# Performance work log

Hardware: AMD Instinct MI355X
Metric: run time of the kernel (lower is better)

## Reference

```python
import jax, jax.numpy as jnp
import numpy as np

C, K, D_LLM = 32, 16, 768
B, L, D_MODEL = 8, 512, 256
H, D_KEYS = 8, 32
TEMP = 1.0 / np.sqrt(D_KEYS)


def setup_inputs() -> dict:
    key = jax.random.key(0)
    ks = jax.random.split(key, 8)
    topk = jax.random.normal(ks[0], (C, K, D_LLM), dtype=jnp.float32)
    ts_emb = jax.random.normal(ks[1], (B, L, D_MODEL), dtype=jnp.float32)
    probs = jax.random.uniform(ks[2], (B, L, C), dtype=jnp.float32)
    probs = probs / jnp.sum(probs, axis=-1, keepdims=True)  # soft cluster probabilities
    scale = 0.02  # keep pre-softmax logits in a stable range
    q_proj = jax.random.normal(ks[3], (C, H * D_KEYS, D_MODEL + 1), dtype=jnp.float32) * scale
    k_proj = jax.random.normal(ks[4], (C, H * D_KEYS, D_LLM + 1), dtype=jnp.float32) * scale
    v_proj = jax.random.normal(ks[5], (C, H * D_KEYS, D_LLM + 1), dtype=jnp.float32) * scale
    out_w = jax.random.normal(ks[6], (C, H, D_KEYS, D_LLM), dtype=jnp.float32) * scale
    out_b = jax.random.normal(ks[7], (C, D_LLM), dtype=jnp.float32) * scale
    return {"topk_token_embeddings": topk, "ts_emb": ts_emb, "cluster_probs": probs,
            "q_proj": q_proj, "k_proj": k_proj, "v_proj": v_proj,
            "out_w": out_w, "out_b": out_b}


def reference(topk_token_embeddings, ts_emb, cluster_probs, q_proj, k_proj, v_proj, out_w, out_b):
    b, l, _ = ts_emb.shape
    c, k, d_llm = topk_token_embeddings.shape
    # per-cluster Q/K/V projections (weights have an extra trailing bias column)
    q = jnp.einsum('bld,cgd->blcg', ts_emb, q_proj[..., :-1]) + q_proj[..., -1]
    q = q.reshape(b, l, c, H, D_KEYS)
    kk = jnp.einsum('ckd,cgd->kcg', topk_token_embeddings, k_proj[..., :-1]) + k_proj[..., -1]
    kk = kk.reshape(k, c, H, D_KEYS)
    v = jnp.einsum('ckd,cgd->kcg', topk_token_embeddings, v_proj[..., :-1]) + v_proj[..., -1]
    v = v.reshape(k, c, H, D_KEYS)
    # cross attention over the k retrieved tokens, per cluster and head
    att = jnp.einsum('blchd,kchd->bchlk', q, kk)  # (B,c,H,L,k)
    att = jax.nn.softmax(TEMP * att, axis=-1)  # dropout disabled (eval)
    out_v = jnp.einsum('bchlk,kchd->bclhd', att, v)
    aligned = jnp.einsum('bclhd,chde->blce', out_v, out_w) + out_b  # (B,L,c,d_llm)
    fused = jnp.sum(aligned * cluster_probs[:, :, :, None], axis=-2)  # (B,L,d_llm)
    return fused
```

## Files before the change

### kernel.cpp

```cpp
#include <hip/hip_runtime.h>
#include <hip/hip_bf16.h>

#define C_   32
#define K_   16
#define DLLM 768
#define DM   256
#define H_   8
#define DK   32
#define G_   256
#define BL   4096
#define NN   4096
#define E_   768
#define LDP  4160
#define TEMPF 0.17677669529663687f
#define SCL2  0.2550348647f

typedef __attribute__((ext_vector_type(8))) short bf16x8;
typedef __attribute__((ext_vector_type(4))) float f32x4;
typedef unsigned int u32;

__device__ __forceinline__ unsigned short f2bf(float f) {
    unsigned int u = __float_as_uint(f);
    unsigned int r = (u + 0x7fffu + ((u >> 16) & 1u)) >> 16;
    return (unsigned short)r;
}
__device__ __forceinline__ float bf2f(unsigned int u) {
    return __uint_as_float(u << 16);
}

__device__ __forceinline__ void gl16(const void* g, void* l) {
    __builtin_amdgcn_global_load_lds(
        (const __attribute__((address_space(1))) u32*)g,
        (__attribute__((address_space(3))) u32*)l, 16, 0, 0);
}

__global__ __launch_bounds__(256) void k1_kv(const float* __restrict__ topk,
                                             const float* __restrict__ kp,
                                             const float* __restrict__ vp,
                                             float* __restrict__ partk,
                                             float* __restrict__ partv) {
    const int c  = blockIdx.x;
    const int dc = blockIdx.y;
    const int d0 = dc * 96;
    const int g  = threadIdx.x;
    __shared__ float t_l[K_][96];
    for (int i = threadIdx.x; i < 384; i += 256) {
        int k = i / 24, c4 = (i % 24) * 4;
        *reinterpret_cast<float4*>(&t_l[k][c4]) =
            *reinterpret_cast<const float4*>(topk + (size_t)(c * K_ + k) * DLLM + d0 + c4);
    }
    __syncthreads();
    const float* kpr = kp + (size_t)(c * G_ + g) * (DLLM + 1) + d0;
    const float* vpr = vp + (size_t)(c * G_ + g) * (DLLM + 1) + d0;
    float acck[K_] = {}, accv[K_] = {};
    for (int d = 0; d < 96; d += 4) {
        float4 wk4 = *reinterpret_cast<const float4*>(kpr + d);
        float4 wv4 = *reinterpret_cast<const float4*>(vpr + d);
        const float wk[4] = {wk4.x, wk4.y, wk4.z, wk4.w};
        const float wv[4] = {wv4.x, wv4.y, wv4.z, wv4.w};
#pragma unroll
        for (int dd = 0; dd < 4; ++dd)
#pragma unroll
            for (int k = 0; k < K_; ++k) {
                acck[k] += wk[dd] * t_l[k][d + dd];
                accv[k] += wv[dd] * t_l[k][d + dd];
            }
    }
    float* pk = partk + ((size_t)(c * 8 + dc) * K_) * G_ + g;
    float* pv = partv + ((size_t)(c * 8 + dc) * K_) * G_ + g;
#pragma unroll
    for (int k = 0; k < K_; ++k) {
        pk[k * G_] = acck[k];
        pv[k * G_] = accv[k];
    }
}

__global__ __launch_bounds__(256) void k1r0(const float* __restrict__ partk,
                                            const float* __restrict__ partv,
                                            const float* __restrict__ kp,
                                            const float* __restrict__ vp,
                                            float* __restrict__ kk,
                                            float* __restrict__ vv,
                                            const float* __restrict__ ts,
                                            const float* __restrict__ probs,
                                            const float* __restrict__ outb,
                                            unsigned short* __restrict__ tsb,
                                            unsigned short* __restrict__ P,
                                            unsigned short* __restrict__ VWt) {
    const int bid0 = blockIdx.x, t = threadIdx.x;
    if (bid0 < 512) {
        const int idx = bid0 * 256 + t;
        const int g = idx & 255, rest = idx >> 8;
        const int k = rest & 15, c = rest >> 4;
        float sk = kp[(size_t)(c * G_ + g) * (DLLM + 1) + DLLM];
        float sv = vp[(size_t)(c * G_ + g) * (DLLM + 1) + DLLM];
#pragma unroll
        for (int dc = 0; dc < 8; ++dc) {
            sk += partk[((size_t)(c * 8 + dc) * K_ + k) * G_ + g];
            sv += partv[((size_t)(c * 8 + dc) * K_ + k) * G_ + g];
        }
        kk[idx] = sk;
        vv[idx] = sv;
        return;
    }
    const int bid = bid0 - 512;
    if (bid < 1024) {
        const int idx = bid * 1024 + t * 4;
        float4 v = *reinterpret_cast<const float4*>(ts + idx);
        uint2 o;
        o.x = f2bf(v.x) | ((unsigned)f2bf(v.y) << 16);
        o.y = f2bf(v.z) | ((unsigned)f2bf(v.w) << 16);
        *reinterpret_cast<uint2*>(tsb + idx) = o;
    } else if (bid < 1056) {
        const int b2 = bid - 1024;
        const int row = b2 * 128 + (t >> 1);
        const int ch = (t & 1) * 16;
        unsigned short o[16];
#pragma unroll
        for (int j = 0; j < 16; ++j) o[j] = f2bf(probs[row * 32 + ch + j]);
        uint4 u0, u1;
        u0.x = o[0] | (o[1] << 16);  u0.y = o[2] | (o[3] << 16);
        u0.z = o[4] | (o[5] << 16);  u0.w = o[6] | (o[7] << 16);
        u1.x = o[8] | (o[9] << 16);  u1.y = o[10] | (o[11] << 16);
        u1.z = o[12] | (o[13] << 16); u1.w = o[14] | (o[15] << 16);
        unsigned short* dst = P + (size_t)row * LDP + 4096 + ch;
        *reinterpret_cast<uint4*>(dst) = u0;
        *reinterpret_cast<uint4*>(dst + 8) = u1;
        uint4 z = {0u, 0u, 0u, 0u};
        unsigned short* pz = P + (size_t)row * LDP + 4128 + ch;
        *reinterpret_cast<uint4*>(pz) = z;
        *reinterpret_cast<uint4*>(pz + 8) = z;
    } else {
        const int idx = (bid - 1056) * 256 + t;
        const int e = idx >> 5, cc = idx & 31;
        VWt[(size_t)e * LDP + 4096 + cc] = f2bf(outb[cc * E_ + e]);
        VWt[(size_t)e * LDP + 4128 + cc] = 0;
    }
}

__global__ __launch_bounds__(768) void k23(const float* __restrict__ qp,
                                           const float* __restrict__ kk,
                                           const float* __restrict__ ow,
                                           const float* __restrict__ vv,
                                           unsigned short* __restrict__ A2t,
                                           float* __restrict__ abias,
                                           unsigned short* __restrict__ VWt) {
    const int c = blockIdx.x, h = blockIdx.y;
    const int t = threadIdx.x;
    __shared__ float kk_l[K_][DK];
    __shared__ float v_l[K_][DK];
    __shared__ float bq_l[DK];
    if (t < 512) {
        int k = t / DK, d = t % DK;
        kk_l[k][d] = kk[(size_t)(c * K_ + k) * G_ + h * DK + d];
        v_l[k][d]  = vv[(size_t)(c * K_ + k) * G_ + h * DK + d];
    }
    if (t < DK)
        bq_l[t] = qp[(size_t)(c * G_ + h * DK + t) * (DM + 1) + DM];
    __syncthreads();
    const int ch = c * H_ + h;
    {
        const int e = t;
        float acc[K_];
#pragma unroll
        for (int k = 0; k < K_; ++k) acc[k] = 0.f;
        for (int d = 0; d < DK; ++d) {
            float w = ow[((size_t)ch * DK + d) * E_ + e];
#pragma unroll
            for (int k = 0; k < K_; ++k) acc[k] += w * v_l[k][d];
        }
#pragma unroll
        for (int k = 0; k < K_; ++k)
            VWt[(size_t)e * LDP + ch * 16 + k] = f2bf(acc[k]);
    }
    if (t < 256) {
        const int m = t;
        float acc[K_];
#pragma unroll
        for (int k = 0; k < K_; ++k) acc[k] = 0.f;
        for (int d = 0; d < DK; ++d) {
            float wq = qp[(size_t)(c * G_ + h * DK + d) * (DM + 1) + m];
#pragma unroll
            for (int k = 0; k < K_; ++k) acc[k] += wq * kk_l[k][d];
        }
#pragma unroll
        for (int k = 0; k < K_; ++k)
            A2t[(size_t)(ch * 16 + k) * DM + m] = f2bf(acc[k] * SCL2);
        if (m < K_) {
            float s = 0.f;
#pragma unroll
            for (int d = 0; d < DK; ++d) s += bq_l[d] * kk_l[m][d];
            abias[ch * 16 + m] = s * SCL2;
        }
    }
}

__global__ __launch_bounds__(256, 2) void k4_att(const unsigned short* __restrict__ A2t,
                                                 const unsigned short* __restrict__ tsb,
                                                 const float* __restrict__ abias,
                                                 const float* __restrict__ probs,
                                                 unsigned short* __restrict__ P) {
    const int n0  = blockIdx.x * 128;
    const int bl0 = blockIdx.y * 256;
    const int t = threadIdx.x;
    const int lane = t & 63, w = t >> 6;
    const int wr = w >> 1, wc = w & 1;
    const int c = lane & 15, g = lane >> 4;
    const int rsl = (c >> 1) & 3;

    __shared__ unsigned short a_l[2][128 * 32];
    __shared__ unsigned short b_l[2][256 * 32];
    __shared__ float ab_l[128];
    __shared__ float pb_l[256];

    if (t < 128) ab_l[t] = abias[n0 + t];
    pb_l[t] = probs[(size_t)(bl0 + t) * C_ + (n0 >> 7)];

    const int srow = t >> 2;
    const int sw = ((t & 3) ^ ((t >> 3) & 3)) * 8;

    f32x4 acc[4][8] = {};

#pragma unroll
    for (int j = 0; j < 2; ++j)
        gl16(A2t + (size_t)(n0 + j * 64 + srow) * DM + sw, &a_l[0][j * 2048 + t * 8]);
#pragma unroll
    for (int j = 0; j < 4; ++j)
        gl16(tsb + (size_t)(bl0 + j * 64 + srow) * DM + sw, &b_l[0][j * 2048 + t * 8]);
    __syncthreads();

    for (int kt = 0; kt < 8; ++kt) {
        const int cur = kt & 1;
        if (kt < 7) {
            const int col = (kt + 1) * 32 + sw;
#pragma unroll
            for (int j = 0; j < 2; ++j)
                gl16(A2t + (size_t)(n0 + j * 64 + srow) * DM + col,
                     &a_l[cur ^ 1][j * 2048 + t * 8]);
#pragma unroll
            for (int j = 0; j < 4; ++j)
                gl16(tsb + (size_t)(bl0 + j * 64 + srow) * DM + col,
                     &b_l[cur ^ 1][j * 2048 + t * 8]);
        }
        bf16x8 af[4], bfr[8];
#pragma unroll
        for (int a = 0; a < 4; ++a)
            af[a] = *reinterpret_cast<const bf16x8*>(
                &a_l[cur][(wr * 64 + a * 16 + c) * 32 + (g ^ rsl) * 8]);
#pragma unroll
        for (int b = 0; b < 8; ++b)
            bfr[b] = *reinterpret_cast<const bf16x8*>(
                &b_l[cur][(wc * 128 + b * 16 + c) * 32 + (g ^ rsl) * 8]);
#pragma unroll
        for (int a = 0; a < 4; ++a)
#pragma unroll
            for (int b = 0; b < 8; ++b)
                acc[a][b] = __builtin_amdgcn_mfma_f32_16x16x32_bf16(af[a], bfr[b], acc[a][b], 0, 0, 0);
        __syncthreads();
    }

#pragma unroll
    for (int a = 0; a < 4; ++a) {
        const int nbase = wr * 64 + a * 16 + g * 4;
#pragma unroll
        for (int b = 0; b < 8; ++b) {
            const int bll = wc * 128 + b * 16 + c;
            float e0 = __builtin_amdgcn_exp2f(acc[a][b][0] + ab_l[nbase + 0]);
            float e1 = __builtin_amdgcn_exp2f(acc[a][b][1] + ab_l[nbase + 1]);
            float e2 = __builtin_amdgcn_exp2f(acc[a][b][2] + ab_l[nbase + 2]);
            float e3 = __builtin_amdgcn_exp2f(acc[a][b][3] + ab_l[nbase + 3]);
            float s = (e0 + e1) + (e2 + e3);
            s += __shfl_xor(s, 16);
            s += __shfl_xor(s, 32);
            const float pv = pb_l[bll] * __builtin_amdgcn_rcpf(s);
            unsigned r0, r1;
            float p0 = e0 * pv, p1 = e1 * pv, p2 = e2 * pv, p3 = e3 * pv;
            asm("v_cvt_pk_bf16_f32 %0, %1, %2" : "=v"(r0) : "v"(p0), "v"(p1));
            asm("v_cvt_pk_bf16_f32 %0, %1, %2" : "=v"(r1) : "v"(p2), "v"(p3));
            uint2 o; o.x = r0; o.y = r1;
            *reinterpret_cast<uint2*>(P + (size_t)(bl0 + bll) * LDP + n0 + nbase) = o;
        }
    }
}

__global__ __launch_bounds__(256, 2) void k5_out(const unsigned short* __restrict__ P,
                                                 const unsigned short* __restrict__ VWt,
                                                 unsigned short* __restrict__ part) {
    const int wg = blockIdx.x;
    const int xcd = wg & 7;
    const int local = wg >> 3;
    const int bl0 = (xcd * 4 + (local & 3)) * 128;
    const int e0  = ((local >> 2) & 3) * 192;
    const int ks  = local >> 4;

    const int t = threadIdx.x;
    const int lane = t & 63, w = t >> 6;
    const int wr = w >> 1, wc = w & 1;
    const int c = lane & 15, g = lane >> 4;
    const int rsl = (c >> 1) & 3;

    __shared__ unsigned short a_l[2][128 * 32];
    __shared__ unsigned short b_l[2][192 * 32];

    const int nstart = ks * 1024;
    const int nsteps = (ks == 3) ? 34 : 32;

    const int srow = t >> 2;
    const int sw = ((t & 3) ^ ((t >> 3) & 3)) * 8;

#pragma unroll
    for (int j = 0; j < 2; ++j)
        gl16(P + (size_t)(bl0 + j * 64 + srow) * LDP + nstart + sw,
             &a_l[0][j * 2048 + t * 8]);
#pragma unroll
    for (int j = 0; j < 3; ++j)
        gl16(VWt + (size_t)(e0 + j * 64 + srow) * LDP + nstart + sw,
             &b_l[0][j * 2048 + t * 8]);
    __syncthreads();

    f32x4 acc[4][6] = {};
    for (int kt = 0; kt < nsteps; ++kt) {
        const int cur = kt & 1;
        if (kt + 1 < nsteps) {
            const int col = nstart + (kt + 1) * 32 + sw;
#pragma unroll
            for (int j = 0; j < 2; ++j)
                gl16(P + (size_t)(bl0 + j * 64 + srow) * LDP + col,
                     &a_l[cur ^ 1][j * 2048 + t * 8]);
#pragma unroll
            for (int j = 0; j < 3; ++j)
                gl16(VWt + (size_t)(e0 + j * 64 + srow) * LDP + col,
                     &b_l[cur ^ 1][j * 2048 + t * 8]);
        }
        bf16x8 af[4], bfr[6];
#pragma unroll
        for (int a = 0; a < 4; ++a)
            af[a] = *reinterpret_cast<const bf16x8*>(
                &a_l[cur][(wr * 64 + a * 16 + c) * 32 + (g ^ rsl) * 8]);
#pragma unroll
        for (int b = 0; b < 6; ++b)
            bfr[b] = *reinterpret_cast<const bf16x8*>(
                &b_l[cur][(wc * 96 + b * 16 + c) * 32 + (g ^ rsl) * 8]);
#pragma unroll
        for (int a = 0; a < 4; ++a)
#pragma unroll
            for (int b = 0; b < 6; ++b)
                acc[a][b] = __builtin_amdgcn_mfma_f32_16x16x32_bf16(af[a], bfr[b], acc[a][b], 0, 0, 0);
        __syncthreads();
    }

    unsigned short* pp = part + ((size_t)ks * BL + bl0) * E_ + e0;
#pragma unroll
    for (int a = 0; a < 4; ++a)
#pragma unroll
        for (int b = 0; b < 6; ++b)
#pragma unroll
            for (int i = 0; i < 4; ++i)
                pp[(size_t)(wr * 64 + a * 16 + g * 4 + i) * E_ + wc * 96 + b * 16 + c] =
                    f2bf(acc[a][b][i]);
}

__global__ __launch_bounds__(256) void k6_red(const unsigned short* __restrict__ part,
                                              float* __restrict__ out) {
    const size_t base = ((size_t)blockIdx.x * 256 + threadIdx.x) * 8;
    float s[8] = {};
#pragma unroll
    for (int ks = 0; ks < 4; ++ks) {
        uint4 v = *reinterpret_cast<const uint4*>(part + (size_t)ks * (BL * E_) + base);
        const unsigned u[4] = {v.x, v.y, v.z, v.w};
#pragma unroll
        for (int j = 0; j < 4; ++j) {
            s[2 * j]     += bf2f(u[j] & 0xffffu);
            s[2 * j + 1] += bf2f(u[j] >> 16);
        }
    }
    *reinterpret_cast<float4*>(out + base)     = make_float4(s[0], s[1], s[2], s[3]);
    *reinterpret_cast<float4*>(out + base + 4) = make_float4(s[4], s[5], s[6], s[7]);
}

extern "C" void kernel_launch(void* const* d_in, const int* in_sizes, int n_in,
                              void* d_out, int out_size, void* d_ws, size_t ws_size,
                              hipStream_t stream) {
    const float* topk  = (const float*)d_in[0];
    const float* ts    = (const float*)d_in[1];
    const float* probs = (const float*)d_in[2];
    const float* qp    = (const float*)d_in[3];
    const float* kp    = (const float*)d_in[4];
    const float* vp    = (const float*)d_in[5];
    const float* ow    = (const float*)d_in[6];
    const float* ob    = (const float*)d_in[7];
    float* out = (float*)d_out;

    char* wp = (char*)d_ws;
    float* kk            = (float*)wp;           wp += 524288;
    float* vv            = (float*)wp;           wp += 524288;
    float* ab            = (float*)wp;           wp += 16384;
    unsigned short* tsb  = (unsigned short*)wp;  wp += 2097152;
    unsigned short* A2t  = (unsigned short*)wp;  wp += 2097152;
    unsigned short* VWt  = (unsigned short*)wp;  wp += (size_t)E_ * LDP * 2;
    unsigned short* P    = (unsigned short*)wp;  wp += (size_t)BL * LDP * 2;
    float* partk         = (float*)wp;           wp += 4194304;
    float* partv         = (float*)wp;           wp += 4194304;
    unsigned short* part = (unsigned short*)wp;

    k1_kv <<<dim3(32, 8),  256, 0, stream>>>(topk, kp, vp, partk, partv);
    k1r0  <<<1664,         256, 0, stream>>>(partk, partv, kp, vp, kk, vv,
                                             ts, probs, ob, tsb, P, VWt);
    k23   <<<dim3(32, 8),  768, 0, stream>>>(qp, kk, ow, vv, A2t, ab, VWt);
    k4_att<<<dim3(32, 16), 256, 0, stream>>>(A2t, tsb, ab, probs, P);
    k5_out<<<512,          256, 0, stream>>>(P, VWt, part);
    k6_red<<<1536,         256, 0, stream>>>(part, out);
}
```

Baseline: 117.9 us.

## Triple-buffer GEMM smem pipelines with vmcnt waits and split KV projection finer

The attention and output GEMM kernels move from double buffering to a three-stage LDS ring. Each iteration now uses one barrier plus explicit s_waitcnt vmcnt counts instead of two __syncthreads, which lets global-to-LDS loads run two tiles ahead. Separately, the K/V projection kernel splits the reduction dimension into 16 chunks instead of 8 to launch more blocks, which doubles the partial-sum buffer and the reduction work in the next kernel. The triple buffer raises LDS use and may lower occupancy, and correctness depends on the hand-set vmcnt values matching the number of loads issued.

```diff
diff --git a/kernel.cpp b/kernel.cpp
--- a/kernel.cpp
+++ b/kernel.cpp
@@ -41,11 +41,11 @@
                                              float* __restrict__ partv) {
     const int c  = blockIdx.x;
     const int dc = blockIdx.y;
-    const int d0 = dc * 96;
+    const int d0 = dc * 48;
     const int g  = threadIdx.x;
-    __shared__ float t_l[K_][96];
-    for (int i = threadIdx.x; i < 384; i += 256) {
-        int k = i / 24, c4 = (i % 24) * 4;
+    __shared__ float t_l[K_][48];
+    if (threadIdx.x < 192) {
+        int k = threadIdx.x / 12, c4 = (threadIdx.x % 12) * 4;
         *reinterpret_cast<float4*>(&t_l[k][c4]) =
             *reinterpret_cast<const float4*>(topk + (size_t)(c * K_ + k) * DLLM + d0 + c4);
     }
@@ -53,7 +53,7 @@
     const float* kpr = kp + (size_t)(c * G_ + g) * (DLLM + 1) + d0;
     const float* vpr = vp + (size_t)(c * G_ + g) * (DLLM + 1) + d0;
     float acck[K_] = {}, accv[K_] = {};
-    for (int d = 0; d < 96; d += 4) {
+    for (int d = 0; d < 48; d += 4) {
         float4 wk4 = *reinterpret_cast<const float4*>(kpr + d);
         float4 wv4 = *reinterpret_cast<const float4*>(vpr + d);
         const float wk[4] = {wk4.x, wk4.y, wk4.z, wk4.w};
@@ -66,8 +66,8 @@
                 accv[k] += wv[dd] * t_l[k][d + dd];
             }
     }
-    float* pk = partk + ((size_t)(c * 8 + dc) * K_) * G_ + g;
-    float* pv = partv + ((size_t)(c * 8 + dc) * K_) * G_ + g;
+    float* pk = partk + ((size_t)(c * 16 + dc) * K_) * G_ + g;
+    float* pv = partv + ((size_t)(c * 16 + dc) * K_) * G_ + g;
 #pragma unroll
     for (int k = 0; k < K_; ++k) {
         pk[k * G_] = acck[k];
@@ -95,9 +95,9 @@
         float sk = kp[(size_t)(c * G_ + g) * (DLLM + 1) + DLLM];
         float sv = vp[(size_t)(c * G_ + g) * (DLLM + 1) + DLLM];
 #pragma unroll
-        for (int dc = 0; dc < 8; ++dc) {
-            sk += partk[((size_t)(c * 8 + dc) * K_ + k) * G_ + g];
-            sv += partv[((size_t)(c * 8 + dc) * K_ + k) * G_ + g];
+        for (int dc = 0; dc < 16; ++dc) {
+            sk += partk[((size_t)(c * 16 + dc) * K_ + k) * G_ + g];
+            sv += partv[((size_t)(c * 16 + dc) * K_ + k) * G_ + g];
         }
         kk[idx] = sk;
         vv[idx] = sv;
@@ -208,8 +208,8 @@
     const int c = lane & 15, g = lane >> 4;
     const int rsl = (c >> 1) & 3;
 
-    __shared__ unsigned short a_l[2][128 * 32];
-    __shared__ unsigned short b_l[2][256 * 32];
+    __shared__ unsigned short a_l[3 * 4096];
+    __shared__ unsigned short b_l[3 * 8192];
     __shared__ float ab_l[128];
     __shared__ float pb_l[256];
 
@@ -219,45 +219,50 @@
     const int srow = t >> 2;
     const int sw = ((t & 3) ^ ((t >> 3) & 3)) * 8;
 
+#define K4_STAGE(buf, kt)                                                         \
+    {                                                                             \
+        const int col_ = (kt) * 32 + sw;                                          \
+        _Pragma("unroll")                                                         \
+        for (int j = 0; j < 2; ++j)                                               \
+            gl16(A2t + (size_t)(n0 + j * 64 + srow) * DM + col_,                  \
+                 &a_l[(buf) * 4096 + j * 2048 + t * 8]);                          \
+        _Pragma("unroll")                                                         \
+        for (int j = 0; j < 4; ++j)                                               \
+            gl16(tsb + (size_t)(bl0 + j * 64 + srow) * DM + col_,                 \
+                 &b_l[(buf) * 8192 + j * 2048 + t * 8]);                          \
+    }
+
+    K4_STAGE(0, 0)
+    K4_STAGE(1, 1)
+    __syncthreads();
+
     f32x4 acc[4][8] = {};
 
 #pragma unroll
-    for (int j = 0; j < 2; ++j)
-        gl16(A2t + (size_t)(n0 + j * 64 + srow) * DM + sw, &a_l[0][j * 2048 + t * 8]);
-#pragma unroll
-    for (int j = 0; j < 4; ++j)
-        gl16(tsb + (size_t)(bl0 + j * 64 + srow) * DM + sw, &b_l[0][j * 2048 + t * 8]);
-    __syncthreads();
-
     for (int kt = 0; kt < 8; ++kt) {
-        const int cur = kt & 1;
-        if (kt < 7) {
-            const int col = (kt + 1) * 32 + sw;
-#pragma unroll
-            for (int j = 0; j < 2; ++j)
-                gl16(A2t + (size_t)(n0 + j * 64 + srow) * DM + col,
-                     &a_l[cur ^ 1][j * 2048 + t * 8]);
-#pragma unroll
-            for (int j = 0; j < 4; ++j)
-                gl16(tsb + (size_t)(bl0 + j * 64 + srow) * DM + col,
-                     &b_l[cur ^ 1][j * 2048 + t * 8]);
-        }
+        const int b0 = kt % 3;
+        const int b2 = (kt + 2) % 3;
+        if (kt > 0) __builtin_amdgcn_s_barrier();
+        if (kt < 6) K4_STAGE(b2, kt + 2)
+        if (kt < 6)      asm volatile("s_waitcnt vmcnt(12)" ::: "memory");
+        else if (kt == 6) asm volatile("s_waitcnt vmcnt(6)" ::: "memory");
+        else              asm volatile("s_waitcnt vmcnt(0)" ::: "memory");
         bf16x8 af[4], bfr[8];
 #pragma unroll
         for (int a = 0; a < 4; ++a)
             af[a] = *reinterpret_cast<const bf16x8*>(
-                &a_l[cur][(wr * 64 + a * 16 + c) * 32 + (g ^ rsl) * 8]);
+                &a_l[b0 * 4096 + (wr * 64 + a * 16 + c) * 32 + (g ^ rsl) * 8]);
 #pragma unroll
         for (int b = 0; b < 8; ++b)
             bfr[b] = *reinterpret_cast<const bf16x8*>(
-                &b_l[cur][(wc * 128 + b * 16 + c) * 32 + (g ^ rsl) * 8]);
+                &b_l[b0 * 8192 + (wc * 128 + b * 16 + c) * 32 + (g ^ rsl) * 8]);
 #pragma unroll
         for (int a = 0; a < 4; ++a)
 #pragma unroll
             for (int b = 0; b < 8; ++b)
                 acc[a][b] = __builtin_amdgcn_mfma_f32_16x16x32_bf16(af[a], bfr[b], acc[a][b], 0, 0, 0);
-        __syncthreads();
-    }
+    }
+#undef K4_STAGE
 
 #pragma unroll
     for (int a = 0; a < 4; ++a) {
@@ -299,8 +304,8 @@
     const int c = lane & 15, g = lane >> 4;
     const int rsl = (c >> 1) & 3;
 
-    __shared__ unsigned short a_l[2][128 * 32];
-    __shared__ unsigned short b_l[2][192 * 32];
+    __shared__ unsigned short a_l[3 * 4096];
+    __shared__ unsigned short b_l[3 * 6144];
 
     const int nstart = ks * 1024;
     const int nsteps = (ks == 3) ? 34 : 32;
@@ -308,46 +313,47 @@
     const int srow = t >> 2;
     const int sw = ((t & 3) ^ ((t >> 3) & 3)) * 8;
 
-#pragma unroll
-    for (int j = 0; j < 2; ++j)
-        gl16(P + (size_t)(bl0 + j * 64 + srow) * LDP + nstart + sw,
-             &a_l[0][j * 2048 + t * 8]);
-#pragma unroll
-    for (int j = 0; j < 3; ++j)
-        gl16(VWt + (size_t)(e0 + j * 64 + srow) * LDP + nstart + sw,
-             &b_l[0][j * 2048 + t * 8]);
-    __syncthreads();
+#define K5_STAGE(buf, kt)                                                         \
+    {                                                                             \
+        const int col_ = nstart + (kt) * 32 + sw;                                 \
+        _Pragma("unroll")                                                         \
+        for (int j = 0; j < 2; ++j)                                               \
+            gl16(P + (size_t)(bl0 + j * 64 + srow) * LDP + col_,                  \
+                 &a_l[(buf) * 4096 + j * 2048 + t * 8]);                          \
+        _Pragma("unroll")                                                         \
+        for (int j = 0; j < 3; ++j)                                               \
+            gl16(VWt + (size_t)(e0 + j * 64 + srow) * LDP + col_,                 \
+                 &b_l[(buf) * 6144 + j * 2048 + t * 8]);                          \
+    }
+
+    K5_STAGE(0, 0)
+    K5_STAGE(1, 1)
 
     f32x4 acc[4][6] = {};
+    int b0 = 0, b1 = 1, b2 = 2;
     for (int kt = 0; kt < nsteps; ++kt) {
-        const int cur = kt & 1;
-        if (kt + 1 < nsteps) {
-            const int col = nstart + (kt + 1) * 32 + sw;
-#pragma unroll
-            for (int j = 0; j < 2; ++j)
-                gl16(P + (size_t)(bl0 + j * 64 + srow) * LDP + col,
-                     &a_l[cur ^ 1][j * 2048 + t * 8]);
-#pragma unroll
-            for (int j = 0; j < 3; ++j)
-                gl16(VWt + (size_t)(e0 + j * 64 + srow) * LDP + col,
-                     &b_l[cur ^ 1][j * 2048 + t * 8]);
-        }
+        if (kt > 0) __builtin_amdgcn_s_barrier();
+        if (kt + 2 < nsteps) K5_STAGE(b2, kt + 2)
+        if (kt + 2 < nsteps)      asm volatile("s_waitcnt vmcnt(10)" ::: "memory");
+        else if (kt + 1 < nsteps) asm volatile("s_waitcnt vmcnt(5)" ::: "memory");
+        else                      asm volatile("s_waitcnt vmcnt(0)" ::: "memory");
         bf16x8 af[4], bfr[6];
 #pragma unroll
         for (int a = 0; a < 4; ++a)
             af[a] = *reinterpret_cast<const bf16x8*>(
-                &a_l[cur][(wr * 64 + a * 16 + c) * 32 + (g ^ rsl) * 8]);
+                &a_l[b0 * 4096 + (wr * 64 + a * 16 + c) * 32 + (g ^ rsl) * 8]);
 #pragma unroll
         for (int b = 0; b < 6; ++b)
             bfr[b] = *reinterpret_cast<const bf16x8*>(
-                &b_l[cur][(wc * 96 + b * 16 + c) * 32 + (g ^ rsl) * 8]);
+                &b_l[b0 * 6144 + (wc * 96 + b * 16 + c) * 32 + (g ^ rsl) * 8]);
 #pragma unroll
         for (int a = 0; a < 4; ++a)
 #pragma unroll
             for (int b = 0; b < 6; ++b)
                 acc[a][b] = __builtin_amdgcn_mfma_f32_16x16x32_bf16(af[a], bfr[b], acc[a][b], 0, 0, 0);
-        __syncthreads();
-    }
+        const int tb = b0; b0 = b1; b1 = b2; b2 = tb;
+    }
+#undef K5_STAGE
 
     unsigned short* pp = part + ((size_t)ks * BL + bl0) * E_ + e0;
 #pragma unroll
@@ -399,11 +405,11 @@
     unsigned short* A2t  = (unsigned short*)wp;  wp += 2097152;
     unsigned short* VWt  = (unsigned short*)wp;  wp += (size_t)E_ * LDP * 2;
     unsigned short* P    = (unsigned short*)wp;  wp += (size_t)BL * LDP * 2;
-    float* partk         = (float*)wp;           wp += 4194304;
-    float* partv         = (float*)wp;           wp += 4194304;
+    float* partk         = (float*)wp;           wp += 8388608;
+    float* partv         = (float*)wp;           wp += 8388608;
     unsigned short* part = (unsigned short*)wp;
 
-    k1_kv <<<dim3(32, 8),  256, 0, stream>>>(topk, kp, vp, partk, partv);
+    k1_kv <<<dim3(32, 16), 256, 0, stream>>>(topk, kp, vp, partk, partv);
     k1r0  <<<1664,         256, 0, stream>>>(partk, partv, kp, vp, kk, vv,
                                              ts, probs, ob, tsb, P, VWt);
     k23   <<<dim3(32, 8),  768, 0, stream>>>(qp, kk, ow, vv, A2t, ab, VWt);
```

New measurement: 137.8 us. 16.9% more time.

## Compute K/V projections in one kernel with wave-level shuffle reductions

Applied to the files above, without the earlier changes.

The K/V projection kernel now loads the full topk tile for a cluster into shared memory. Each wave computes complete dot products over all 768 features for four output rows, reducing across lanes with xor shuffles and adding the bias directly. This removes the partial-sum buffers and the separate reduction pass, and the remaining conversion work moves into its own smaller kernel. The price is a 48KB shared tile per block and many shuffle operations, which may limit occupancy.

```diff
diff --git a/kernel.cpp b/kernel.cpp
--- a/kernel.cpp
+++ b/kernel.cpp
@@ -37,73 +37,67 @@
 __global__ __launch_bounds__(256) void k1_kv(const float* __restrict__ topk,
                                              const float* __restrict__ kp,
                                              const float* __restrict__ vp,
-                                             float* __restrict__ partk,
-                                             float* __restrict__ partv) {
+                                             float* __restrict__ kk,
+                                             float* __restrict__ vv) {
     const int c  = blockIdx.x;
-    const int dc = blockIdx.y;
-    const int d0 = dc * 96;
-    const int g  = threadIdx.x;
-    __shared__ float t_l[K_][96];
-    for (int i = threadIdx.x; i < 384; i += 256) {
-        int k = i / 24, c4 = (i % 24) * 4;
-        *reinterpret_cast<float4*>(&t_l[k][c4]) =
-            *reinterpret_cast<const float4*>(topk + (size_t)(c * K_ + k) * DLLM + d0 + c4);
+    const int gq = blockIdx.y;
+    const int t = threadIdx.x;
+    const int lane = t & 63, w = t >> 6;
+
+    __shared__ float t_l[K_][DLLM];
+    {
+        const float4* src = reinterpret_cast<const float4*>(topk + (size_t)c * K_ * DLLM);
+        float4* dst = reinterpret_cast<float4*>(&t_l[0][0]);
+#pragma unroll
+        for (int i = 0; i < 12; ++i)
+            dst[t + i * 256] = src[t + i * 256];
     }
     __syncthreads();
-    const float* kpr = kp + (size_t)(c * G_ + g) * (DLLM + 1) + d0;
-    const float* vpr = vp + (size_t)(c * G_ + g) * (DLLM + 1) + d0;
-    float acck[K_] = {}, accv[K_] = {};
-    for (int d = 0; d < 96; d += 4) {
-        float4 wk4 = *reinterpret_cast<const float4*>(kpr + d);
-        float4 wv4 = *reinterpret_cast<const float4*>(vpr + d);
-        const float wk[4] = {wk4.x, wk4.y, wk4.z, wk4.w};
-        const float wv[4] = {wv4.x, wv4.y, wv4.z, wv4.w};
-#pragma unroll
-        for (int dd = 0; dd < 4; ++dd)
+
+#pragma unroll
+    for (int gi = 0; gi < 4; ++gi) {
+        const int g = gq * 16 + w * 4 + gi;
+        const float* kpr = kp + (size_t)(c * G_ + g) * (DLLM + 1);
+        const float* vpr = vp + (size_t)(c * G_ + g) * (DLLM + 1);
+        const float bk = kpr[DLLM], bv = vpr[DLLM];
+        float acck[K_] = {}, accv[K_] = {};
+#pragma unroll
+        for (int r = 0; r < 3; ++r) {
+            const int d = r * 256 + lane * 4;
+            float4 wk = *reinterpret_cast<const float4*>(kpr + d);
+            float4 wv = *reinterpret_cast<const float4*>(vpr + d);
 #pragma unroll
             for (int k = 0; k < K_; ++k) {
-                acck[k] += wk[dd] * t_l[k][d + dd];
-                accv[k] += wv[dd] * t_l[k][d + dd];
+                float4 t4 = *reinterpret_cast<const float4*>(&t_l[k][d]);
+                acck[k] += wk.x * t4.x + wk.y * t4.y + wk.z * t4.z + wk.w * t4.w;
+                accv[k] += wv.x * t4.x + wv.y * t4.y + wv.z * t4.z + wv.w * t4.w;
             }
-    }
-    float* pk = partk + ((size_t)(c * 8 + dc) * K_) * G_ + g;
-    float* pv = partv + ((size_t)(c * 8 + dc) * K_) * G_ + g;
-#pragma unroll
-    for (int k = 0; k < K_; ++k) {
-        pk[k * G_] = acck[k];
-        pv[k * G_] = accv[k];
-    }
-}
-
-__global__ __launch_bounds__(256) void k1r0(const float* __restrict__ partk,
-                                            const float* __restrict__ partv,
-                                            const float* __restrict__ kp,
-                                            const float* __restrict__ vp,
-                                            float* __restrict__ kk,
-                                            float* __restrict__ vv,
-                                            const float* __restrict__ ts,
-                                            const float* __restrict__ probs,
-                                            const float* __restrict__ outb,
-                                            unsigned short* __restrict__ tsb,
-                                            unsigned short* __restrict__ P,
-                                            unsigned short* __restrict__ VWt) {
-    const int bid0 = blockIdx.x, t = threadIdx.x;
-    if (bid0 < 512) {
-        const int idx = bid0 * 256 + t;
-        const int g = idx & 255, rest = idx >> 8;
-        const int k = rest & 15, c = rest >> 4;
-        float sk = kp[(size_t)(c * G_ + g) * (DLLM + 1) + DLLM];
-        float sv = vp[(size_t)(c * G_ + g) * (DLLM + 1) + DLLM];
-#pragma unroll
-        for (int dc = 0; dc < 8; ++dc) {
-            sk += partk[((size_t)(c * 8 + dc) * K_ + k) * G_ + g];
-            sv += partv[((size_t)(c * 8 + dc) * K_ + k) * G_ + g];
-        }
-        kk[idx] = sk;
-        vv[idx] = sv;
-        return;
-    }
-    const int bid = bid0 - 512;
+        }
+#pragma unroll
+        for (int s = 32; s >= 1; s >>= 1) {
+#pragma unroll
+            for (int k = 0; k < K_; ++k) {
+                acck[k] += __shfl_xor(acck[k], s);
+                accv[k] += __shfl_xor(accv[k], s);
+            }
+        }
+        if (lane == 0) {
+#pragma unroll
+            for (int k = 0; k < K_; ++k) {
+                kk[(size_t)(c * K_ + k) * G_ + g] = acck[k] + bk;
+                vv[(size_t)(c * K_ + k) * G_ + g] = accv[k] + bv;
+            }
+        }
+    }
+}
+
+__global__ __launch_bounds__(256) void k0_cvt(const float* __restrict__ ts,
+                                              const float* __restrict__ probs,
+                                              const float* __restrict__ outb,
+                                              unsigned short* __restrict__ tsb,
+                                              unsigned short* __restrict__ P,
+                                              unsigned short* __restrict__ VWt) {
+    const int bid = blockIdx.x, t = threadIdx.x;
     if (bid < 1024) {
         const int idx = bid * 1024 + t * 4;
         float4 v = *reinterpret_cast<const float4*>(ts + idx);
@@ -399,13 +393,10 @@
     unsigned short* A2t  = (unsigned short*)wp;  wp += 2097152;
     unsigned short* VWt  = (unsigned short*)wp;  wp += (size_t)E_ * LDP * 2;
     unsigned short* P    = (unsigned short*)wp;  wp += (size_t)BL * LDP * 2;
-    float* partk         = (float*)wp;           wp += 4194304;
-    float* partv         = (float*)wp;           wp += 4194304;
     unsigned short* part = (unsigned short*)wp;
 
-    k1_kv <<<dim3(32, 8),  256, 0, stream>>>(topk, kp, vp, partk, partv);
-    k1r0  <<<1664,         256, 0, stream>>>(partk, partv, kp, vp, kk, vv,
-                                             ts, probs, ob, tsb, P, VWt);
+    k1_kv <<<dim3(32, 16), 256, 0, stream>>>(topk, kp, vp, kk, vv);
+    k0_cvt<<<1152,         256, 0, stream>>>(ts, probs, ob, tsb, P, VWt);
     k23   <<<dim3(32, 8),  768, 0, stream>>>(qp, kk, ow, vv, A2t, ab, VWt);
     k4_att<<<dim3(32, 16), 256, 0, stream>>>(A2t, tsb, ab, probs, P);
     k5_out<<<512,          256, 0, stream>>>(P, VWt, part);
```

Measured after the change: 115.3 us. -2.2%, faster.
